# Kernel tuning notes

Measured on AMD Instinct MI355X. Metric: run time of the kernel, lower is better.

Reference implementation:

```python
import jax, jax.numpy as jnp
import numpy as np

B, N, DIM, H, DH = 4, 4096, 1024, 16, 64
INNER = H * DH


def setup_inputs() -> dict:
    key = jax.random.key(0)
    k1, k2, k3, k4 = jax.random.split(key, 4)
    x = jax.random.normal(k1, (B, N, DIM), dtype=jnp.float32)
    mask = jax.random.randint(k2, (B, N), 0, 2).astype(bool)
    Wqkv = jax.random.normal(k3, (DIM, 3 * INNER), dtype=jnp.float32) * (DIM ** -0.5)
    Wout = jax.random.normal(k4, (INNER, DIM), dtype=jnp.float32) * (INNER ** -0.5)
    bout = jnp.zeros((DIM,), dtype=jnp.float32)
    return {"x": x, "mask": mask, "Wqkv": Wqkv, "Wout": Wout, "bout": bout}


def _split_heads(t):
    b, n, _ = t.shape
    return t.reshape(b, n, H, DH).transpose(0, 2, 1, 3)  # b h n d


def reference(x, mask, Wqkv, Wout, bout):
    qkv = x @ Wqkv                      # [b, n, 3*inner]
    q, k, v = jnp.split(qkv, 3, axis=-1)
    q, k, v = map(_split_heads, (q, k, v))  # [b, h, n, d]
    q = jax.nn.elu(q) + 1.0
    k = jax.nn.elu(k) + 1.0
    m = mask[:, None, :, None]          # [b, 1, n, 1]
    k = jnp.where(m, k, 0.0)
    v = jnp.where(m, v, 0.0)
    kv = jnp.einsum('bhnd,bhne->bhde', k, v)      # [b, h, d, d]
    out = jnp.einsum('bhnd,bhde->bhne', q, kv)    # [b, h, n, d]
    z = 1.0 / (jnp.einsum('bhnd,bhd->bhn', q, k.sum(axis=2)) + 1e-6)
    out = out * z[..., None]
    out = out.transpose(0, 2, 1, 3).reshape(x.shape[0], -1, INNER)  # [b, n, inner]
    return out @ Wout + bout
```

## Files before the change

kernel.cpp:

```cpp
#include <hip/hip_runtime.h>
#include <hip/hip_bf16.h>
#include <cstddef>
#include <cstdint>

#define B_     4
#define N_     4096
#define DIM_   1024
#define H_     16
#define DH_    64
#define INNER_ 1024
#define MTOK   (B_ * N_)
#define QKVC   (3 * INNER_)
#define NCH    16
#define CHUNK  (N_ / NCH)

typedef __attribute__((ext_vector_type(8))) short short8;
typedef __attribute__((ext_vector_type(4))) float f32x4;

__device__ __forceinline__ float elu1(float x) {
    return x > 0.f ? x + 1.f : __expf(x);
}
__device__ __forceinline__ unsigned short f2bf(float f) {
    __hip_bfloat16 h = __float2bfloat16(f);
    return __builtin_bit_cast(unsigned short, h);
}
__device__ __forceinline__ float bf2f(unsigned short u) {
    __hip_bfloat16 h = __builtin_bit_cast(__hip_bfloat16, u);
    return __bfloat162float(h);
}

__device__ __forceinline__ void gload16(const void* g, void* l) {
    __builtin_amdgcn_global_load_lds(
        (const __attribute__((address_space(1))) unsigned int*)g,
        (__attribute__((address_space(3))) unsigned int*)l, 16, 0, 0);
}

__global__ __launch_bounds__(256) void prep_fused(
    const float* __restrict__ x, unsigned short* __restrict__ xbf,
    const float* __restrict__ Wqkv, unsigned short* __restrict__ wqkvT,
    const float* __restrict__ Wout, unsigned short* __restrict__ woutT)
{
    __shared__ float t[32][33];
    const int blk = blockIdx.x;
    if (blk < 2048) {
        const long n8 = (long)MTOK * DIM_ / 8;
        const long stride = 2048L * 256;
        for (long i = (long)blk * 256 + threadIdx.x; i < n8; i += stride) {
            const float4 f0 = reinterpret_cast<const float4*>(x)[2 * i];
            const float4 f1 = reinterpret_cast<const float4*>(x)[2 * i + 1];
            short8 u;
            u[0] = (short)f2bf(f0.x); u[1] = (short)f2bf(f0.y);
            u[2] = (short)f2bf(f0.z); u[3] = (short)f2bf(f0.w);
            u[4] = (short)f2bf(f1.x); u[5] = (short)f2bf(f1.y);
            u[6] = (short)f2bf(f1.z); u[7] = (short)f2bf(f1.w);
            reinterpret_cast<short8*>(xbf)[i] = u;
        }
        return;
    }
    const float* src; unsigned short* dst; int R, C, r0, c0;
    if (blk < 5120) {
        const int id = blk - 2048;
        src = Wqkv; dst = wqkvT; R = DIM_; C = QKVC;
        r0 = (id & 31) * 32; c0 = (id >> 5) * 32;
    } else {
        const int id = blk - 5120;
        src = Wout; dst = woutT; R = INNER_; C = INNER_;
        r0 = (id & 31) * 32; c0 = (id >> 5) * 32;
    }
    const int tx = threadIdx.x & 31, ty = threadIdx.x >> 5;
#pragma unroll
    for (int i = 0; i < 4; ++i)
        t[ty * 4 + i][tx] = src[(size_t)(r0 + ty * 4 + i) * C + c0 + tx];
    __syncthreads();
#pragma unroll
    for (int i = 0; i < 4; ++i)
        dst[(size_t)(c0 + ty * 4 + i) * R + r0 + tx] = f2bf(t[tx][ty * 4 + i]);
}

template<int EPI, int HAS_BIAS>
__global__ __launch_bounds__(512, 2) void gemm256(
    const unsigned short* __restrict__ A,
    const unsigned short* __restrict__ BT,
    void* __restrict__ Cv,
    const float* __restrict__ bias,
    const int* __restrict__ msk,
    int M, int N, int K, int lda, int ldb, int ldc)
{
    __shared__ __align__(16) unsigned short smem[4][256 * 64];

    const int tid = threadIdx.x;
    const int wv  = tid >> 6;
    const int ln  = tid & 63;
    const int wr  = wv >> 2;
    const int wc  = wv & 3;

    const int nwg = gridDim.x;
    int wg = blockIdx.x;
    {
        const int q = nwg >> 3, r = nwg & 7;
        const int xcd = wg & 7, lid = wg >> 3;
        wg = (xcd < r ? xcd * (q + 1) : r * (q + 1) + (xcd - r) * q) + lid;
    }
    const int ncol = N >> 8;
    const int bx = wg % ncol;
    const int by = wg / ncol;
    const int row0 = by << 8;
    const int col0 = bx << 8;

    const int l8    = ln >> 3;
    const int sslot = ((ln & 7) ^ l8) << 3;

    const int lr16 = ln & 15;
    const int kc   = ln >> 4;
    const int sw   = lr16 & 7;
    const int soff0 = (kc ^ sw) << 3;
    const int soff1 = ((4 + kc) ^ sw) << 3;

    f32x4 acc[8][4];
#pragma unroll
    for (int m = 0; m < 8; ++m)
#pragma unroll
        for (int n = 0; n < 4; ++n) acc[m][n] = f32x4{0.f, 0.f, 0.f, 0.f};

    const int NT = K >> 6;

#pragma unroll
    for (int i = 0; i < 4; ++i) {
        const int lr = wv * 32 + i * 8;
        gload16(&A [(size_t)(row0 + lr + l8) * lda + sslot], &smem[0][lr * 64]);
        gload16(&BT[(size_t)(col0 + lr + l8) * ldb + sslot], &smem[2][lr * 64]);
    }
    __syncthreads();

    for (int t = 0; t < NT; ++t) {
        const int cur = t & 1;
        const unsigned short* bufA = smem[cur];
        const unsigned short* bufB = smem[2 + cur];
        short8 bf[4][2];
        short8 af[2][2][2];

#pragma unroll
        for (int n = 0; n < 4; ++n) {
            const int row = wc * 64 + n * 16 + lr16;
            bf[n][0] = *reinterpret_cast<const short8*>(&bufB[row * 64 + soff0]);
            bf[n][1] = *reinterpret_cast<const short8*>(&bufB[row * 64 + soff1]);
        }
#pragma unroll
        for (int mi = 0; mi < 2; ++mi) {
            const int row = wr * 128 + mi * 16 + lr16;
            af[0][mi][0] = *reinterpret_cast<const short8*>(&bufA[row * 64 + soff0]);
            af[0][mi][1] = *reinterpret_cast<const short8*>(&bufA[row * 64 + soff1]);
        }
        if (t + 1 < NT) {
            const int k0 = (t + 1) << 6;
            unsigned short* nA = smem[cur ^ 1];
            unsigned short* nB = smem[2 + (cur ^ 1)];
#pragma unroll
            for (int i = 0; i < 4; ++i) {
                const int lr = wv * 32 + i * 8;
                gload16(&A [(size_t)(row0 + lr + l8) * lda + k0 + sslot],
                        &nA[lr * 64]);
                gload16(&BT[(size_t)(col0 + lr + l8) * ldb + k0 + sslot],
                        &nB[lr * 64]);
            }
        }

#pragma unroll
        for (int p = 0; p < 4; ++p) {
            if (p > 0) __builtin_amdgcn_s_barrier();
            if (p < 3) {
#pragma unroll
                for (int mi = 0; mi < 2; ++mi) {
                    const int row = wr * 128 + ((p + 1) * 2 + mi) * 16 + lr16;
                    af[(p + 1) & 1][mi][0] =
                        *reinterpret_cast<const short8*>(&bufA[row * 64 + soff0]);
                    af[(p + 1) & 1][mi][1] =
                        *reinterpret_cast<const short8*>(&bufA[row * 64 + soff1]);
                }
            }
            __builtin_amdgcn_s_setprio(1);
#pragma unroll
            for (int mi = 0; mi < 2; ++mi)
#pragma unroll
                for (int n = 0; n < 4; ++n) {
                    acc[p * 2 + mi][n] = __builtin_amdgcn_mfma_f32_16x16x32_bf16(
                        af[p & 1][mi][0], bf[n][0], acc[p * 2 + mi][n], 0, 0, 0);
                    acc[p * 2 + mi][n] = __builtin_amdgcn_mfma_f32_16x16x32_bf16(
                        af[p & 1][mi][1], bf[n][1], acc[p * 2 + mi][n], 0, 0, 0);
                }
            __builtin_amdgcn_s_setprio(0);
        }
        __syncthreads();
    }

    const int orow = (ln >> 4) << 2;
    const int ocol = ln & 15;

    if constexpr (EPI == 2) {
        unsigned short* tb = &smem[0][0];
#pragma unroll
        for (int m = 0; m < 8; ++m) {
            const int rrb = wr * 128 + m * 16 + orow;
            const int4 m4 = *reinterpret_cast<const int4*>(&msk[row0 + rrb]);
            int mv[4] = { m4.x, m4.y, m4.z, m4.w };
            const int slot16 = rrb >> 3, half = (rrb >> 2) & 1;
#pragma unroll
            for (int n = 0; n < 4; ++n) {
                const int chl = wc * 64 + n * 16 + ocol;
                const bool isk = (col0 + chl) < 1024;
                ushort4 st;
#pragma unroll
                for (int r2 = 0; r2 < 4; ++r2) {
                    float o = acc[m][n][r2];
                    o = mv[r2] ? (isk ? elu1(o) : o) : 0.f;
                    ((unsigned short*)&st)[r2] = f2bf(o);
                }
                *reinterpret_cast<ushort4*>(
                    &tb[chl * 256 + ((slot16 ^ (chl & 7)) << 3) + half * 4]) = st;
            }
        }
        __syncthreads();
        unsigned short* dst = (unsigned short*)Cv;
#pragma unroll
        for (int i = 0; i < 16; ++i) {
            const int idx = i * 512 + tid;
            const int ch = idx >> 5;
            const int sl = idx & 31;
            const short8 v = *reinterpret_cast<const short8*>(
                &tb[ch * 256 + ((sl ^ (ch & 7)) << 3)]);
            *reinterpret_cast<short8*>(
                &dst[(size_t)(col0 + ch) * ldc + row0 + sl * 8]) = v;
        }
    } else {
#pragma unroll
        for (int m = 0; m < 8; ++m) {
            const int rrb = row0 + wr * 128 + m * 16 + orow;
#pragma unroll
            for (int n = 0; n < 4; ++n) {
                const int c = col0 + wc * 64 + n * 16 + ocol;
                float bv = 0.f;
                if constexpr (HAS_BIAS) bv = bias[c];
#pragma unroll
                for (int r2 = 0; r2 < 4; ++r2) {
                    const int rr = rrb + r2;
                    float o = acc[m][n][r2] + bv;
                    if constexpr (EPI == 1) {
                        o = elu1(o);
                        ((unsigned short*)Cv)[(size_t)rr * ldc + c] = f2bf(o);
                    } else {
                        ((float*)Cv)[(size_t)rr * ldc + c] = o;
                    }
                }
            }
        }
    }
}

__global__ __launch_bounds__(256) void kv_partial(
    const unsigned short* __restrict__ kvT, float* __restrict__ part)
{
    const int bh = blockIdx.x;
    const int ch = blockIdx.y;
    const int b = bh / H_, h = bh % H_;
    const int tok0 = b * N_ + ch * CHUNK;

    __shared__ __align__(16) unsigned short kt[64 * 64];
    __shared__ __align__(16) unsigned short vt[64 * 64];
    __shared__ float ksr[4][64];

    const int tid = threadIdx.x;
    const int wv = tid >> 6, ln = tid & 63;
    const int wr = wv >> 1, wc = wv & 1;
    const int l8 = ln >> 3;
    const int sslot = ((ln & 7) ^ l8) << 3;
    const int lr16 = ln & 15;
    const int kc = ln >> 4;
    const int sw = lr16 & 7;

    const size_t krow = (size_t)(h * 64) * MTOK;
    const size_t vrow = (size_t)(1024 + h * 64) * MTOK;

    f32x4 acc[2][2];
#pragma unroll
    for (int i = 0; i < 2; ++i)
#pragma unroll
        for (int j = 0; j < 2; ++j) acc[i][j] = f32x4{0.f, 0.f, 0.f, 0.f};

    const int kd = tid & 63, kq = tid >> 6;
    float ksacc = 0.f;

    for (int st = 0; st < 4; ++st) {
        const int tb = tok0 + st * 64;
        __syncthreads();
#pragma unroll
        for (int i = 0; i < 2; ++i) {
            const int rb = (wv * 2 + i) * 8;
            gload16(&kvT[krow + (size_t)(rb + l8) * MTOK + tb + sslot], &kt[rb * 64]);
            gload16(&kvT[vrow + (size_t)(rb + l8) * MTOK + tb + sslot], &vt[rb * 64]);
        }
        __syncthreads();
#pragma unroll
        for (int ks = 0; ks < 2; ++ks) {
            const int soff = ((ks * 4 + kc) ^ sw) << 3;
            short8 af[2], bf[2];
#pragma unroll
            for (int mi = 0; mi < 2; ++mi)
                af[mi] = *reinterpret_cast<const short8*>(
                    &kt[(wr * 32 + mi * 16 + lr16) * 64 + soff]);
#pragma unroll
            for (int ni = 0; ni < 2; ++ni)
                bf[ni] = *reinterpret_cast<const short8*>(
                    &vt[(wc * 32 + ni * 16 + lr16) * 64 + soff]);
#pragma unroll
            for (int mi = 0; mi < 2; ++mi)
#pragma unroll
                for (int ni = 0; ni < 2; ++ni)
                    acc[mi][ni] = __builtin_amdgcn_mfma_f32_16x16x32_bf16(
                        af[mi], bf[ni], acc[mi][ni], 0, 0, 0);
        }
#pragma unroll
        for (int sl = 0; sl < 2; ++sl) {
            const int phys = (kq * 2 + sl) ^ (kd & 7);
            short8 v = *reinterpret_cast<const short8*>(&kt[kd * 64 + phys * 8]);
#pragma unroll
            for (int e = 0; e < 8; ++e) ksacc += bf2f((unsigned short)v[e]);
        }
    }
    ksr[kq][kd] = ksacc;
    __syncthreads();

    float* p = part + ((size_t)bh * NCH + ch) * 4160;
    const int orow = (ln >> 4) << 2;
    const int ocol = ln & 15;
#pragma unroll
    for (int mi = 0; mi < 2; ++mi)
#pragma unroll
        for (int ni = 0; ni < 2; ++ni) {
            const int d0 = wr * 32 + mi * 16 + orow;
            const int e  = wc * 32 + ni * 16 + ocol;
#pragma unroll
            for (int r = 0; r < 4; ++r)
                p[(d0 + r) * 64 + e] = acc[mi][ni][r];
        }
    if (tid < 64)
        p[4096 + tid] = ksr[0][tid] + ksr[1][tid] + ksr[2][tid] + ksr[3][tid];
}

__global__ __launch_bounds__(256) void kv_reduce(
    const float* __restrict__ part, unsigned short* __restrict__ kvtb,
    float* __restrict__ ksumf)
{
    const int bh = blockIdx.x;
    for (int idx = threadIdx.x; idx < 4096; idx += 256) {
        float s = 0.f;
        for (int c = 0; c < NCH; ++c)
            s += part[((size_t)bh * NCH + c) * 4160 + idx];
        const int d = idx >> 6, e = idx & 63;
        const unsigned short hi = f2bf(s);
        const float lo = s - bf2f(hi);
        kvtb[(size_t)bh * 8192 + e * 64 + d] = hi;
        kvtb[(size_t)bh * 8192 + 4096 + e * 64 + d] = f2bf(lo);
    }
    if (threadIdx.x < 64) {
        float s = 0.f;
        for (int c = 0; c < NCH; ++c)
            s += part[((size_t)bh * NCH + c) * 4160 + 4096 + threadIdx.x];
        ksumf[bh * 64 + threadIdx.x] = s;
    }
}

__global__ __launch_bounds__(256) void attn_mfma(
    const unsigned short* __restrict__ qbf,
    const unsigned short* __restrict__ kvtb,
    const float* __restrict__ ksumf,
    unsigned short* __restrict__ attnbf)
{
    const int bh = blockIdx.x, tt = blockIdx.y;
    const int b = bh / H_, h = bh % H_;
    const int tok0 = b * N_ + tt * 256;

    __shared__ __align__(16) unsigned short qt[256 * 64];
    __shared__ float den[256];

    const int tid = threadIdx.x;
    const int wv = tid >> 6, ln = tid & 63;
    const int l8 = ln >> 3;
    const int sslot = ((ln & 7) ^ l8) << 3;
    const int lr16 = ln & 15;
    const int kc = ln >> 4;

    const unsigned short* kvb = kvtb + (size_t)bh * 8192;
    short8 bhf[4][2], blf[4][2];
#pragma unroll
    for (int n = 0; n < 4; ++n)
#pragma unroll
        for (int ks = 0; ks < 2; ++ks) {
            const int off = (n * 16 + lr16) * 64 + ks * 32 + kc * 8;
            bhf[n][ks] = *reinterpret_cast<const short8*>(&kvb[off]);
            blf[n][ks] = *reinterpret_cast<const short8*>(&kvb[4096 + off]);
        }

#pragma unroll
    for (int i = 0; i < 8; ++i) {
        const int rb = wv * 64 + i * 8;
        gload16(&qbf[(size_t)(tok0 + rb + l8) * INNER_ + h * 64 + sslot],
                &qt[rb * 64]);
    }

    {
        float dsum = 0.f;
        const unsigned short* qr = &qbf[(size_t)(tok0 + tid) * INNER_ + h * 64];
        const float* ksp = &ksumf[bh * 64];
#pragma unroll
        for (int j = 0; j < 8; ++j) {
            short8 v = *reinterpret_cast<const short8*>(&qr[j * 8]);
#pragma unroll
            for (int e = 0; e < 8; ++e)
                dsum += bf2f((unsigned short)v[e]) * ksp[j * 8 + e];
        }
        den[tid] = dsum;
    }
    __syncthreads();

    f32x4 acc[4][4];
#pragma unroll
    for (int m = 0; m < 4; ++m)
#pragma unroll
        for (int n = 0; n < 4; ++n) acc[m][n] = f32x4{0.f, 0.f, 0.f, 0.f};

#pragma unroll
    for (int ks = 0; ks < 2; ++ks) {
        const int soff = ((ks * 4 + kc) ^ (lr16 & 7)) << 3;
        short8 af[4];
#pragma unroll
        for (int m = 0; m < 4; ++m)
            af[m] = *reinterpret_cast<const short8*>(
                &qt[(wv * 64 + m * 16 + lr16) * 64 + soff]);
#pragma unroll
        for (int m = 0; m < 4; ++m)
#pragma unroll
            for (int n = 0; n < 4; ++n) {
                acc[m][n] = __builtin_amdgcn_mfma_f32_16x16x32_bf16(
                    af[m], bhf[n][ks], acc[m][n], 0, 0, 0);
                acc[m][n] = __builtin_amdgcn_mfma_f32_16x16x32_bf16(
                    af[m], blf[n][ks], acc[m][n], 0, 0, 0);
            }
    }

    const int orow = (ln >> 4) << 2;
    const int ocol = ln & 15;
#pragma unroll
    for (int m = 0; m < 4; ++m) {
        const int rl = wv * 64 + m * 16 + orow;
#pragma unroll
        for (int r = 0; r < 4; ++r) {
            const float z = 1.f / (den[rl + r] + 1e-6f);
            const size_t orow_g = (size_t)(tok0 + rl + r) * INNER_ + h * 64;
#pragma unroll
            for (int n = 0; n < 4; ++n)
                attnbf[orow_g + n * 16 + ocol] = f2bf(acc[m][n][r] * z);
        }
    }
}

extern "C" void kernel_launch(void* const* d_in, const int* in_sizes, int n_in,
                              void* d_out, int out_size, void* d_ws, size_t ws_size,
                              hipStream_t stream)
{
    const float* x    = (const float*)d_in[0];
    const int*   mask = (const int*)d_in[1];
    const float* Wqkv = (const float*)d_in[2];
    const float* Wout = (const float*)d_in[3];
    const float* bout = (const float*)d_in[4];
    float* out = (float*)d_out;

    const size_t need = 127156224;
    if (ws_size < need) return;

    char* base = (char*)d_ws;
    unsigned short* xbf    = (unsigned short*)base;
    unsigned short* attnbf = xbf;
    unsigned short* kvT    = (unsigned short*)(base + 33554432);
    unsigned short* wqkvT  = (unsigned short*)(base + 100663296);
    unsigned short* woutT  = (unsigned short*)(base + 106954752);
    float* part  = (float*)(base + 109051904);
    unsigned short* kvtb = (unsigned short*)(base + 126091264);
    float* ksumf = (float*)(base + 127139840);
    unsigned short* qbf = (unsigned short*)d_out;

    prep_fused<<<dim3(6144), dim3(256), 0, stream>>>(
        x, xbf, Wqkv, wqkvT, Wout, woutT);

    gemm256<1, 0><<<dim3(64 * 4), dim3(512), 0, stream>>>(
        xbf, wqkvT, qbf, nullptr, nullptr, MTOK, 1024, DIM_, DIM_, DIM_, 1024);
    gemm256<2, 0><<<dim3(64 * 8), dim3(512), 0, stream>>>(
        xbf, wqkvT + (size_t)1024 * 1024, kvT, nullptr, mask,
        MTOK, 2048, DIM_, DIM_, DIM_, MTOK);

    kv_partial<<<dim3(B_ * H_, NCH), dim3(256), 0, stream>>>(kvT, part);
    kv_reduce<<<dim3(B_ * H_), dim3(256), 0, stream>>>(part, kvtb, ksumf);

    attn_mfma<<<dim3(B_ * H_, N_ / 256), dim3(256), 0, stream>>>(
        qbf, kvtb, ksumf, attnbf);

    gemm256<0, 1><<<dim3(64 * 4), dim3(512), 0, stream>>>(
        attnbf, woutT, out, bout, nullptr,
        MTOK, INNER_, INNER_, INNER_, INNER_, INNER_);
}
```

Before: 237.7 us.

## Restructure GEMM mainloop into 8-phase quadrant pipeline with half-tile staged loads

Restructures the 256x256 GEMM tile into four 128x128 quadrants computed in four phases per K-step, with A/B half-tiles loaded into eight LDS buffers in a staged schedule interleaved between phases. Explicit vmcnt/lgkmcnt waits, s_barriers and sched_barriers replace the prior whole-tile double buffering. The goal is to overlap global->LDS loads and LDS reads with MFMA work more finely and to reduce stalls. The risks are more barriers per K-step and the hand-tuned wait counts, which could be wrong or could serialize the work.

Result: no change. 240.0 us (+1.0%).

```diff
diff --git a/kernel.cpp b/kernel.cpp
--- a/kernel.cpp
+++ b/kernel.cpp
@@ -34,6 +34,10 @@
         (const __attribute__((address_space(1))) unsigned int*)g,
         (__attribute__((address_space(3))) unsigned int*)l, 16, 0, 0);
 }
+
+#define SBAR() __builtin_amdgcn_sched_barrier(0)
+#define WBAR() __builtin_amdgcn_s_barrier()
+#define LGK0() asm volatile("s_waitcnt lgkmcnt(0)" ::: "memory")
 
 __global__ __launch_bounds__(256) void prep_fused(
     const float* __restrict__ x, unsigned short* __restrict__ xbf,
@@ -78,7 +82,7 @@
 }
 
 template<int EPI, int HAS_BIAS>
-__global__ __launch_bounds__(512, 2) void gemm256(
+__global__ __launch_bounds__(512, 2) void gemm8p(
     const unsigned short* __restrict__ A,
     const unsigned short* __restrict__ BT,
     void* __restrict__ Cv,
@@ -86,13 +90,13 @@
     const int* __restrict__ msk,
     int M, int N, int K, int lda, int ldb, int ldc)
 {
-    __shared__ __align__(16) unsigned short smem[4][256 * 64];
+    __shared__ __align__(16) unsigned short smem[8][128 * 64];
 
     const int tid = threadIdx.x;
     const int wv  = tid >> 6;
     const int ln  = tid & 63;
-    const int wr  = wv >> 2;
-    const int wc  = wv & 3;
+    const int wr2 = wv >> 2;
+    const int wc2 = wv & 3;
 
     const int nwg = gridDim.x;
     int wg = blockIdx.x;
@@ -116,82 +120,111 @@
     const int soff0 = (kc ^ sw) << 3;
     const int soff1 = ((4 + kc) ^ sw) << 3;
 
-    f32x4 acc[8][4];
-#pragma unroll
-    for (int m = 0; m < 8; ++m)
-#pragma unroll
-        for (int n = 0; n < 4; ++n) acc[m][n] = f32x4{0.f, 0.f, 0.f, 0.f};
+    f32x4 acc[2][2][4][2];
+#pragma unroll
+    for (int a = 0; a < 2; ++a)
+#pragma unroll
+        for (int b = 0; b < 2; ++b)
+#pragma unroll
+            for (int c = 0; c < 4; ++c)
+#pragma unroll
+                for (int d = 0; d < 2; ++d)
+                    acc[a][b][c][d] = f32x4{0.f, 0.f, 0.f, 0.f};
 
     const int NT = K >> 6;
-
-#pragma unroll
-    for (int i = 0; i < 4; ++i) {
-        const int lr = wv * 32 + i * 8;
-        gload16(&A [(size_t)(row0 + lr + l8) * lda + sslot], &smem[0][lr * 64]);
-        gload16(&BT[(size_t)(col0 + lr + l8) * ldb + sslot], &smem[2][lr * 64]);
-    }
-    __syncthreads();
+    const int NH = NT << 2;
+
+    auto stage = [&](int I) {
+        if (I >= NH) return;
+        const int TI = I >> 2, j = I & 3;
+        const int hf = j >> 1;
+        const bool isA = (j == 0) || (j == 3);
+        unsigned short* dst = isA ? &smem[(TI & 1) * 2 + hf][0]
+                                  : &smem[4 + (TI & 1) * 2 + hf][0];
+#pragma unroll
+        for (int i = 0; i < 2; ++i) {
+            const int rbase = (wv * 2 + i) * 8;
+            if (isA)
+                gload16(&A[(size_t)(row0 + hf * 128 + rbase + l8) * lda
+                           + TI * 64 + sslot], dst + rbase * 64);
+            else
+                gload16(&BT[(size_t)(col0 + hf * 128 + rbase + l8) * ldb
+                            + TI * 64 + sslot], dst + rbase * 64);
+        }
+    };
+    auto readA = [&](short8 (&af)[4][2], int buf, int Qm) {
+        const unsigned short* p = &smem[buf * 2 + Qm][0];
+#pragma unroll
+        for (int mi = 0; mi < 4; ++mi) {
+            const int row = wr2 * 64 + mi * 16 + lr16;
+            af[mi][0] = *reinterpret_cast<const short8*>(&p[row * 64 + soff0]);
+            af[mi][1] = *reinterpret_cast<const short8*>(&p[row * 64 + soff1]);
+        }
+    };
+    auto readB = [&](short8 (&bq)[2][2], int buf, int Qn) {
+        const unsigned short* p = &smem[4 + buf * 2 + Qn][0];
+#pragma unroll
+        for (int ni = 0; ni < 2; ++ni) {
+            const int row = wc2 * 32 + ni * 16 + lr16;
+            bq[ni][0] = *reinterpret_cast<const short8*>(&p[row * 64 + soff0]);
+            bq[ni][1] = *reinterpret_cast<const short8*>(&p[row * 64 + soff1]);
+        }
+    };
+
+#define MMAC(QM, QN, BQ)                                                       \
+    do {                                                                       \
+        __builtin_amdgcn_s_setprio(1);                                         \
+        _Pragma("unroll")                                                      \
+        for (int mi = 0; mi < 4; ++mi) {                                       \
+            _Pragma("unroll")                                                  \
+            for (int ni = 0; ni < 2; ++ni) {                                   \
+                acc[QM][QN][mi][ni] = __builtin_amdgcn_mfma_f32_16x16x32_bf16( \
+                    af[mi][0], BQ[ni][0], acc[QM][QN][mi][ni], 0, 0, 0);       \
+                acc[QM][QN][mi][ni] = __builtin_amdgcn_mfma_f32_16x16x32_bf16( \
+                    af[mi][1], BQ[ni][1], acc[QM][QN][mi][ni], 0, 0, 0);       \
+            }                                                                  \
+        }                                                                      \
+        __builtin_amdgcn_s_setprio(0);                                         \
+    } while (0)
+
+#pragma unroll
+    for (int I = 0; I < 7; ++I) stage(I);
+    asm volatile("s_waitcnt vmcnt(6)" ::: "memory");
+    WBAR(); SBAR();
 
     for (int t = 0; t < NT; ++t) {
-        const int cur = t & 1;
-        const unsigned short* bufA = smem[cur];
-        const unsigned short* bufB = smem[2 + cur];
-        short8 bf[4][2];
-        short8 af[2][2][2];
-
-#pragma unroll
-        for (int n = 0; n < 4; ++n) {
-            const int row = wc * 64 + n * 16 + lr16;
-            bf[n][0] = *reinterpret_cast<const short8*>(&bufB[row * 64 + soff0]);
-            bf[n][1] = *reinterpret_cast<const short8*>(&bufB[row * 64 + soff1]);
-        }
-#pragma unroll
-        for (int mi = 0; mi < 2; ++mi) {
-            const int row = wr * 128 + mi * 16 + lr16;
-            af[0][mi][0] = *reinterpret_cast<const short8*>(&bufA[row * 64 + soff0]);
-            af[0][mi][1] = *reinterpret_cast<const short8*>(&bufA[row * 64 + soff1]);
-        }
-        if (t + 1 < NT) {
-            const int k0 = (t + 1) << 6;
-            unsigned short* nA = smem[cur ^ 1];
-            unsigned short* nB = smem[2 + (cur ^ 1)];
-#pragma unroll
-            for (int i = 0; i < 4; ++i) {
-                const int lr = wv * 32 + i * 8;
-                gload16(&A [(size_t)(row0 + lr + l8) * lda + k0 + sslot],
-                        &nA[lr * 64]);
-                gload16(&BT[(size_t)(col0 + lr + l8) * ldb + k0 + sslot],
-                        &nB[lr * 64]);
-            }
-        }
-
-#pragma unroll
-        for (int p = 0; p < 4; ++p) {
-            if (p > 0) __builtin_amdgcn_s_barrier();
-            if (p < 3) {
-#pragma unroll
-                for (int mi = 0; mi < 2; ++mi) {
-                    const int row = wr * 128 + ((p + 1) * 2 + mi) * 16 + lr16;
-                    af[(p + 1) & 1][mi][0] =
-                        *reinterpret_cast<const short8*>(&bufA[row * 64 + soff0]);
-                    af[(p + 1) & 1][mi][1] =
-                        *reinterpret_cast<const short8*>(&bufA[row * 64 + soff1]);
-                }
-            }
-            __builtin_amdgcn_s_setprio(1);
-#pragma unroll
-            for (int mi = 0; mi < 2; ++mi)
-#pragma unroll
-                for (int n = 0; n < 4; ++n) {
-                    acc[p * 2 + mi][n] = __builtin_amdgcn_mfma_f32_16x16x32_bf16(
-                        af[p & 1][mi][0], bf[n][0], acc[p * 2 + mi][n], 0, 0, 0);
-                    acc[p * 2 + mi][n] = __builtin_amdgcn_mfma_f32_16x16x32_bf16(
-                        af[p & 1][mi][1], bf[n][1], acc[p * 2 + mi][n], 0, 0, 0);
-                }
-            __builtin_amdgcn_s_setprio(0);
-        }
-        __syncthreads();
-    }
+        const int buf = t & 1;
+        const int sI = (t << 2) + 7;
+        short8 af[4][2], bq[2][2][2];
+
+        readA(af, buf, 0);
+        readB(bq[0], buf, 0);
+        stage(sI);
+        SBAR(); WBAR(); LGK0(); SBAR();
+        MMAC(0, 0, bq[0]);
+        SBAR(); WBAR(); SBAR();
+
+        readB(bq[1], buf, 1);
+        stage(sI + 1);
+        SBAR(); WBAR(); LGK0(); SBAR();
+        MMAC(0, 1, bq[1]);
+        SBAR(); WBAR(); SBAR();
+
+        readA(af, buf, 1);
+        stage(sI + 2);
+        SBAR(); WBAR(); LGK0(); SBAR();
+        MMAC(1, 1, bq[1]);
+        SBAR(); WBAR(); SBAR();
+
+        stage(sI + 3);
+        SBAR(); WBAR(); SBAR();
+        MMAC(1, 0, bq[0]);
+        SBAR();
+        if (t < NT - 2) asm volatile("s_waitcnt vmcnt(6)" ::: "memory");
+        else            asm volatile("s_waitcnt vmcnt(0)" ::: "memory");
+        WBAR(); SBAR();
+    }
+#undef MMAC
 
     const int orow = (ln >> 4) << 2;
     const int ocol = ln & 15;
@@ -199,19 +232,23 @@
     if constexpr (EPI == 2) {
         unsigned short* tb = &smem[0][0];
 #pragma unroll
-        for (int m = 0; m < 8; ++m) {
-            const int rrb = wr * 128 + m * 16 + orow;
+        for (int Qm = 0; Qm < 2; ++Qm)
+#pragma unroll
+        for (int mi = 0; mi < 4; ++mi) {
+            const int rrb = Qm * 128 + wr2 * 64 + mi * 16 + orow;
             const int4 m4 = *reinterpret_cast<const int4*>(&msk[row0 + rrb]);
             int mv[4] = { m4.x, m4.y, m4.z, m4.w };
             const int slot16 = rrb >> 3, half = (rrb >> 2) & 1;
 #pragma unroll
-            for (int n = 0; n < 4; ++n) {
-                const int chl = wc * 64 + n * 16 + ocol;
+            for (int Qn = 0; Qn < 2; ++Qn)
+#pragma unroll
+            for (int ni = 0; ni < 2; ++ni) {
+                const int chl = Qn * 128 + wc2 * 32 + ni * 16 + ocol;
                 const bool isk = (col0 + chl) < 1024;
                 ushort4 st;
 #pragma unroll
                 for (int r2 = 0; r2 < 4; ++r2) {
-                    float o = acc[m][n][r2];
+                    float o = acc[Qm][Qn][mi][ni][r2];
                     o = mv[r2] ? (isk ? elu1(o) : o) : 0.f;
                     ((unsigned short*)&st)[r2] = f2bf(o);
                 }
@@ -233,17 +270,21 @@
         }
     } else {
 #pragma unroll
-        for (int m = 0; m < 8; ++m) {
-            const int rrb = row0 + wr * 128 + m * 16 + orow;
-#pragma unroll
-            for (int n = 0; n < 4; ++n) {
-                const int c = col0 + wc * 64 + n * 16 + ocol;
+        for (int Qm = 0; Qm < 2; ++Qm)
+#pragma unroll
+        for (int mi = 0; mi < 4; ++mi) {
+            const int rrb = row0 + Qm * 128 + wr2 * 64 + mi * 16 + orow;
+#pragma unroll
+            for (int Qn = 0; Qn < 2; ++Qn)
+#pragma unroll
+            for (int ni = 0; ni < 2; ++ni) {
+                const int c = col0 + Qn * 128 + wc2 * 32 + ni * 16 + ocol;
                 float bv = 0.f;
                 if constexpr (HAS_BIAS) bv = bias[c];
 #pragma unroll
                 for (int r2 = 0; r2 < 4; ++r2) {
                     const int rr = rrb + r2;
-                    float o = acc[m][n][r2] + bv;
+                    float o = acc[Qm][Qn][mi][ni][r2] + bv;
                     if constexpr (EPI == 1) {
                         o = elu1(o);
                         ((unsigned short*)Cv)[(size_t)rr * ldc + c] = f2bf(o);
@@ -491,9 +532,9 @@
     prep_fused<<<dim3(6144), dim3(256), 0, stream>>>(
         x, xbf, Wqkv, wqkvT, Wout, woutT);
 
-    gemm256<1, 0><<<dim3(64 * 4), dim3(512), 0, stream>>>(
+    gemm8p<1, 0><<<dim3(64 * 4), dim3(512), 0, stream>>>(
         xbf, wqkvT, qbf, nullptr, nullptr, MTOK, 1024, DIM_, DIM_, DIM_, 1024);
-    gemm256<2, 0><<<dim3(64 * 8), dim3(512), 0, stream>>>(
+    gemm8p<2, 0><<<dim3(64 * 8), dim3(512), 0, stream>>>(
         xbf, wqkvT + (size_t)1024 * 1024, kvT, nullptr, mask,
         MTOK, 2048, DIM_, DIM_, DIM_, MTOK);
 
@@ -503,7 +544,7 @@
     attn_mfma<<<dim3(B_ * H_, N_ / 256), dim3(256), 0, stream>>>(
         qbf, kvtb, ksumf, attnbf);
 
-    gemm256<0, 1><<<dim3(64 * 4), dim3(512), 0, stream>>>(
+    gemm8p<0, 1><<<dim3(64 * 4), dim3(512), 0, stream>>>(
         attnbf, woutT, out, bout, nullptr,
         MTOK, INNER_, INNER_, INNER_, INNER_, INNER_);
 }
```
